# Kernel optimization log

Hardware: AMD Instinct MI355X
Metric: run time of the kernel (lower is better)

Reference implementation:

```python
import jax, jax.numpy as jnp
import numpy as np

C = 1024        # number of classes
N = 8           # proxies per class
ALLNUM = C * N  # 8192 total proxies
DIM = 512
R = 0.05
TOPK = int(np.ceil(R * ALLNUM))  # 410
LAM = 0.3
B = 2048


def setup_inputs() -> dict:
    key = jax.random.key(0)
    k1, k2, k3 = jax.random.split(key, 3)
    inp = jax.random.normal(k1, (B, DIM), dtype=jnp.float32)
    target = jax.random.randint(k2, (B,), 0, C, dtype=jnp.int64)
    # kaiming-uniform-initialized proxies approximated by scaled normal init
    proxies = jax.random.normal(k3, (DIM, ALLNUM), dtype=jnp.float32)
    instance_label = jnp.repeat(jnp.arange(C, dtype=jnp.int64), N)  # [ALLNUM]
    return {"input": inp, "target": target, "Proxies": proxies,
            "instance_label": instance_label}


def reference(input, target, Proxies, instance_label):
    # L2-normalize each proxy column (F.normalize along dim=0, eps=1e-12)
    norm = jnp.maximum(jnp.linalg.norm(Proxies, axis=0, keepdims=True), 1e-12)
    centers = Proxies / norm                             # [DIM, ALLNUM]
    similarity = input @ centers                          # [B, ALLNUM]

    positive_mask = (target[:, None] == instance_label[None, :]).astype(similarity.dtype)
    _, indices = jax.lax.top_k(similarity + 1000.0 * positive_mask, TOPK)  # [B, TOPK]

    rows = jnp.arange(similarity.shape[0])[:, None]
    mask = jnp.zeros_like(similarity).at[rows, indices].set(1.0)
    prob_a = mask * similarity                            # sparse-masked similarities

    y_instance_onehot = jax.nn.one_hot(instance_label, C, dtype=similarity.dtype)  # [ALLNUM, C]
    logits = prob_a @ y_instance_onehot                   # [B, C]

    y_target_onehot = jax.nn.one_hot(target, C, dtype=similarity.dtype)  # [B, C]
    logits_mask = 1.0 - (logits == 0.0).astype(similarity.dtype)

    # scale_mask_softmax with scale=1 along dim=1
    e = jnp.exp(logits) * logits_mask
    predict = e / (1e-8 + jnp.sum(e, axis=1, keepdims=True))
    lossClassify = jnp.mean(jnp.sum(-y_target_onehot * jnp.log(predict + 1e-20), axis=1))

    # proxy regularizer: cross-entropy of proxy-vs-class logits
    simCenter = centers.T @ centers                       # [ALLNUM, ALLNUM]
    centers_logits = simCenter @ y_instance_onehot        # [ALLNUM, C]
    logp = jax.nn.log_softmax(centers_logits, axis=1)
    reg = -jnp.mean(jnp.take_along_axis(logp, instance_label[:, None], axis=1))

    return (lossClassify + LAM * reg, lossClassify)
```

## Files before the change

### kernel.cpp

```cpp
#include <hip/hip_runtime.h>
#include <hip/hip_bf16.h>
#include <math.h>

#define C_CLS   1024
#define NPROXY  8
#define ALLNUM  8192
#define DIM     512
#define TOPK    410
#define LAM     0.3f
#define BATCH   2048

typedef __bf16 bf16x8 __attribute__((ext_vector_type(8)));
typedef float floatx4 __attribute__((ext_vector_type(4)));
typedef unsigned short ushort_t;

#define WS_RNORM 0
#define WS_SIG   8192
#define WS_LP    10240
#define WS_RSE   12288
#define WS_DIAG  20480
#define WS_ABF   28672
#define WS_PBF   552960
#define WS_STBF  2650112
#define WS_SIMBF 2912256

__device__ inline float block_reduce(float v, int is_max, float* red, int t) {
    #pragma unroll
    for (int o = 32; o > 0; o >>= 1) {
        float w = __shfl_down(v, o);
        v = is_max ? fmaxf(v, w) : (v + w);
    }
    __syncthreads();
    if ((t & 63) == 0) red[t >> 6] = v;
    __syncthreads();
    return is_max ? fmaxf(fmaxf(red[0], red[1]), fmaxf(red[2], red[3]))
                  : (red[0] + red[1] + red[2] + red[3]);
}

__device__ inline ushort_t f2bf(float f) {
    unsigned u = __float_as_uint(f);
    return (ushort_t)((u + 0x7FFFu + ((u >> 16) & 1u)) >> 16);
}

__device__ inline void ld_g2l_16(const void* g, void* l) {
    __builtin_amdgcn_global_load_lds(
        (const __attribute__((address_space(1))) unsigned int*)g,
        (__attribute__((address_space(3))) unsigned int*)l,
        16, 0, 0);
}

__device__ inline unsigned f2ord(float f) {
    unsigned u = __float_as_uint(f);
    return (u & 0x80000000u) ? ~u : (u | 0x80000000u);
}

__global__ __launch_bounds__(256) void k_prep1(const float* __restrict__ P,
                                               const float* __restrict__ input,
                                               float* __restrict__ rnorm,
                                               float* __restrict__ rowsig,
                                               float* __restrict__ rse,
                                               ushort_t* __restrict__ Abf,
                                               ushort_t* __restrict__ Pbf) {
    __shared__ float tile[32][33];
    float* cred = &tile[0][0];
    int bx = blockIdx.x, t = threadIdx.x;
    if (bx < 256) {
        int tc = t & 31, g = t >> 5;
        int c = bx * 32 + tc;
        const float* pc = P + (size_t)(g * 64) * ALLNUM + c;
        float s = 0.f;
        #pragma unroll 8
        for (int d = 0; d < 64; ++d) {
            float v = pc[(size_t)d * ALLNUM];
            s += v * v;
        }
        cred[g * 32 + tc] = s;
        int gid = bx * 256 + t;
        if (gid < 8192) rse[gid] = 0.f;
        __syncthreads();
        if (g == 0) {
            float tot = 0.f;
            #pragma unroll
            for (int k = 0; k < 8; ++k) tot += cred[k * 32 + tc];
            rnorm[c] = 1.0f / fmaxf(sqrtf(tot), 1e-12f);
        }
    } else if (bx < 256 + 1024) {
        int a = bx - 256;
        int idx = a * 256 + t;
        float4 v = ((const float4*)input)[idx];
        ushort4 o;
        o.x = f2bf(v.x); o.y = f2bf(v.y); o.z = f2bf(v.z); o.w = f2bf(v.w);
        ((ushort4*)Abf)[idx] = o;
        float sq = v.x * v.x + v.y * v.y + v.z * v.z + v.w * v.w;
        #pragma unroll
        for (int off = 32; off > 0; off >>= 1) sq += __shfl_down(sq, off);
        int lane = t & 63, w = t >> 6;
        if (lane == 0) cred[w] = sq;
        __syncthreads();
        if (t == 0) {
            rowsig[2 * a]     = sqrtf(cred[0] + cred[1]);
            rowsig[2 * a + 1] = sqrtf(cred[2] + cred[3]);
        }
    } else {
        int id = bx - 1280;
        int c0 = (id & 255) * 32, r0 = (id >> 8) * 32;
        int tc = t & 31, tr = t >> 5;
        #pragma unroll
        for (int p = 0; p < 4; ++p)
            tile[tr + p * 8][tc] = P[(size_t)(r0 + tr + p * 8) * ALLNUM + c0 + tc];
        __syncthreads();
        #pragma unroll
        for (int p = 0; p < 4; ++p) {
            int oc = tr + p * 8;
            Pbf[(size_t)(c0 + oc) * DIM + r0 + tc] = f2bf(tile[tc][oc]);
        }
    }
}

__global__ __launch_bounds__(256) void k_stage2(const ushort_t* __restrict__ A,
                                                const ushort_t* __restrict__ B,
                                                const float* __restrict__ P,
                                                const float* __restrict__ rnorm,
                                                ushort_t* __restrict__ simbf,
                                                ushort_t* __restrict__ Stbf) {
    __shared__ __align__(16) ushort_t smem[2 * 128 * 64];
    int bx = blockIdx.x, t = threadIdx.x;

    if (bx < 1024) {
        ushort_t* sA = smem;
        ushort_t* sB = smem + 128 * 64;
        int w = t >> 6, lane = t & 63;
        int wm = w >> 1, wn = w & 1;
        int bj = (bx & 63) * 128, bi = (bx >> 6) * 128;

        floatx4 acc[4][4];
        #pragma unroll
        for (int tm = 0; tm < 4; ++tm)
            #pragma unroll
            for (int tn = 0; tn < 4; ++tn)
                acc[tm][tn] = (floatx4){0.f, 0.f, 0.f, 0.f};

        for (int k0 = 0; k0 < DIM; k0 += 64) {
            #pragma unroll
            for (int it = 0; it < 4; ++it) {
                int c = w * 256 + it * 64 + lane;
                int m = c >> 3, s = c & 7;
                int q = s ^ (m & 7);
                ld_g2l_16(A + ((size_t)(bi + m) << 9) + k0 + q * 8,
                          &sA[(w * 256 + it * 64) * 8]);
            }
            #pragma unroll
            for (int it = 0; it < 4; ++it) {
                int c = w * 256 + it * 64 + lane;
                int m = c >> 3, s = c & 7;
                int q = s ^ (m & 7);
                ld_g2l_16(B + ((size_t)(bj + m) << 9) + k0 + q * 8,
                          &sB[(w * 256 + it * 64) * 8]);
            }
            asm volatile("s_waitcnt vmcnt(0)" ::: "memory");
            __syncthreads();

            #pragma unroll
            for (int kk = 0; kk < 2; ++kk) {
                bf16x8 af[4], bfr[4];
                int ml = lane & 15, q = lane >> 4;
                #pragma unroll
                for (int tm = 0; tm < 4; ++tm) {
                    int m = wm * 64 + tm * 16 + ml;
                    int s = (kk * 4 + q) ^ (m & 7);
                    af[tm] = *(const bf16x8*)&sA[m * 64 + s * 8];
                }
                #pragma unroll
                for (int tn = 0; tn < 4; ++tn) {
                    int n = wn * 64 + tn * 16 + ml;
                    int s = (kk * 4 + q) ^ (n & 7);
                    bfr[tn] = *(const bf16x8*)&sB[n * 64 + s * 8];
                }
                #pragma unroll
                for (int tm = 0; tm < 4; ++tm)
                    #pragma unroll
                    for (int tn = 0; tn < 4; ++tn)
                        acc[tm][tn] = __builtin_amdgcn_mfma_f32_16x16x32_bf16(
                            af[tm], bfr[tn], acc[tm][tn], 0, 0, 0);
            }
            __syncthreads();
        }

        int ml = lane & 15, qd = lane >> 4;
        #pragma unroll
        for (int tm = 0; tm < 4; ++tm) {
            int rowb = bi + wm * 64 + tm * 16 + qd * 4;
            #pragma unroll
            for (int tn = 0; tn < 4; ++tn) {
                int col = bj + wn * 64 + tn * 16 + ml;
                float sc = rnorm[col];
                #pragma unroll
                for (int i = 0; i < 4; ++i)
                    simbf[(size_t)(rowb + i) * ALLNUM + col] = f2bf(acc[tm][tn][i] * sc);
            }
        }
    } else {
        float* tile = (float*)smem;
        int id = bx - 1024;
        int c0 = (id & 31) * 32, d0 = (id >> 5) * 32;
        int cl = t & 31, dl8 = t >> 5;
        #pragma unroll
        for (int p = 0; p < 4; ++p) {
            int d = d0 + dl8 + 8 * p;
            int c = c0 + cl;
            const float* pp = P + (size_t)d * ALLNUM + c * NPROXY;
            const float* rn = rnorm + c * NPROXY;
            float4 a = *(const float4*)pp;
            float4 b = *(const float4*)(pp + 4);
            float4 ra = *(const float4*)rn;
            float4 rb = *(const float4*)(rn + 4);
            tile[(dl8 + 8 * p) * 33 + cl] =
                a.x * ra.x + a.y * ra.y + a.z * ra.z + a.w * ra.w +
                b.x * rb.x + b.y * rb.y + b.z * rb.z + b.w * rb.w;
        }
        __syncthreads();
        #pragma unroll
        for (int p = 0; p < 4; ++p) {
            int cl2 = dl8 + 8 * p, dl2 = t & 31;
            Stbf[(size_t)(c0 + cl2) * DIM + d0 + dl2] = f2bf(tile[dl2 * 33 + cl2]);
        }
    }
}

#define SEL_CAP 1024
#define GCAP    64

__device__ inline void suffix_select1(unsigned* s_hist, unsigned kk,
                                      unsigned* s_wtot, unsigned* sh_bin,
                                      unsigned* sh_k, int t, int lane, int wid) {
    unsigned h = s_hist[t];
    unsigned v = h;
    #pragma unroll
    for (int off = 1; off < 64; off <<= 1) {
        unsigned o = __shfl_down(v, off);
        if (lane + off < 64) v += o;
    }
    if (lane == 0) s_wtot[wid] = v;
    __syncthreads();
    unsigned above = v - h;
    for (int w2 = wid + 1; w2 < 4; ++w2) above += s_wtot[w2];
    unsigned cum = above + h;
    if (cum >= kk && above < kk) { *sh_bin = (unsigned)t; *sh_k = kk - above; }
    __syncthreads();
}

__global__ __launch_bounds__(256) void k_stage3(const ushort_t* __restrict__ simbf,
                                                const int* __restrict__ target,
                                                const float* __restrict__ rowsig,
                                                float* __restrict__ loss_part,
                                                const ushort_t* __restrict__ Pbf,
                                                const ushort_t* __restrict__ Stbf,
                                                const float* __restrict__ rnorm,
                                                float* __restrict__ rse,
                                                float* __restrict__ diag) {
    __shared__ __align__(16) unsigned char smem[16384];
    int bx = blockIdx.x, t = threadIdx.x;
    int lane = t & 63, wid = t >> 6;

    if (bx < 2048) {
        float*    s_cls  = (float*)smem;
        float*    s_bval = (float*)(smem + 4096);
        ushort_t* s_bcol = (ushort_t*)(smem + 8192);
        unsigned* s_bhist= (unsigned*)(smem + 10240);
        float*    s_gval = (float*)(smem + 11264);
        unsigned* s_wtot = (unsigned*)(smem + 11520);
        unsigned* shv    = (unsigned*)(smem + 11536);
        float*    shf    = (float*)(smem + 11552);
        int*      shi    = (int*)(smem + 11556);
        float*    red    = (float*)(smem + 11568);

        int b = bx;
        const ushort_t* row = simbf + (size_t)b * ALLNUM;
        int tgt = target[b];
        float sig = rowsig[b] * (1.0f / 22.616f);
        float hiT = 1.80f * sig, loT = 1.47f * sig;
        float binscale = 256.0f / (hiT - loT);

        uint4 r4[4];
        #pragma unroll
        for (int p = 0; p < 4; ++p) r4[p] = ((const uint4*)row)[t + 256 * p];
        float f[4][8];
        #pragma unroll
        for (int p = 0; p < 4; ++p) {
            const unsigned* u = (const unsigned*)&r4[p];
            #pragma unroll
            for (int k = 0; k < 4; ++k) {
                f[p][2 * k]     = __uint_as_float(u[k] << 16);
                f[p][2 * k + 1] = __uint_as_float(u[k] & 0xFFFF0000u);
            }
        }

        if (t == 0) { shv[0] = 0; shv[1] = 0; }
        s_bhist[t] = 0;
        __syncthreads();

        float ndef = 0.f;
        #pragma unroll
        for (int p = 0; p < 4; ++p) {
            int cls = t + 256 * p;
            if (cls == tgt) {
                float s8 = f[p][0] + f[p][1] + f[p][2] + f[p][3] +
                           f[p][4] + f[p][5] + f[p][6] + f[p][7];
                s_cls[cls] = s8;
            } else {
                float ds = 0.f;
                #pragma unroll
                for (int e = 0; e < 8; ++e) {
                    float v = f[p][e];
                    if (v >= hiT) { ds += v; ndef += 1.f; }
                    else if (v >= loT) {
                        unsigned idx = atomicAdd(&shv[0], 1u);
                        if (idx < SEL_CAP) { s_bval[idx] = v; s_bcol[idx] = (ushort_t)(cls * 8 + e); }
                        int bin = (int)((v - loT) * binscale);
                        bin = (bin > 255) ? 255 : bin;
                        atomicAdd(&s_bhist[bin], 1u);
                    }
                }
                s_cls[cls] = ds;
            }
        }
        float ndefT = block_reduce(ndef, 0, red, t);
        int bc = (int)shv[0];
        int kq = (TOPK - NPROXY) - (int)ndefT;
        if (t == 0) shi[0] = (kq < 0 || bc < kq || bc > SEL_CAP) ? 1 : 0;
        __syncthreads();

        if (!shi[0]) {
            if (kq > 0) {
                suffix_select1(s_bhist, (unsigned)kq, s_wtot, &shv[2], &shv[3], t, lane, wid);
                int B = (int)shv[2];
                int knew = (int)shv[3];
                for (int j = t; j < bc; j += 256) {
                    float v = s_bval[j];
                    int bin = (int)((v - loT) * binscale);
                    bin = (bin > 255) ? 255 : bin;
                    if (bin == B) {
                        unsigned g = atomicAdd(&shv[1], 1u);
                        if (g < GCAP) s_gval[g] = v;
                    }
                }
                __syncthreads();
                int gc = (int)shv[1];
                if (gc <= GCAP) {
                    if (t < gc) {
                        float vj = s_gval[t];
                        unsigned g = 0, geq = 0;
                        for (int i = 0; i < gc; ++i) {
                            float vi = s_gval[i];
                            g   += (vi > vj) ? 1u : 0u;
                            geq += (vi >= vj) ? 1u : 0u;
                        }
                        if (g < (unsigned)knew && geq >= (unsigned)knew) shf[0] = vj;
                    }
                } else {
                    for (int j = t; j < bc; j += 256) {
                        float vj = s_bval[j];
                        unsigned g = 0, geq = 0;
                        for (int i = 0; i < bc; ++i) {
                            float vi = s_bval[i];
                            g   += (vi > vj) ? 1u : 0u;
                            geq += (vi >= vj) ? 1u : 0u;
                        }
                        if (g < (unsigned)kq && geq >= (unsigned)kq) shf[0] = vj;
                    }
                }
                __syncthreads();
                float thr = shf[0];
                for (int j = t; j < bc; j += 256)
                    if (s_bval[j] >= thr)
                        atomicAdd(&s_cls[s_bcol[j] >> 3], s_bval[j]);
            }
        } else {
            unsigned L = 0u, R = 0xFFFFFFFFu;
            for (int it = 0; it < 33 && R - L > 1; ++it) {
                unsigned mid = L + ((R - L) >> 1);
                float c = 0.f;
                #pragma unroll
                for (int p = 0; p < 4; ++p) {
                    int cls = t + 256 * p;
                    if (cls != tgt) {
                        #pragma unroll
                        for (int e = 0; e < 8; ++e)
                            c += (f2ord(f[p][e]) >= mid) ? 1.f : 0.f;
                    }
                }
                c = block_reduce(c, 0, red, t);
                if (c >= (float)(TOPK - NPROXY)) L = mid; else R = mid;
                __syncthreads();
            }
            #pragma unroll
            for (int p = 0; p < 4; ++p) {
                int cls = t + 256 * p;
                if (cls != tgt) {
                    float s = 0.f;
                    #pragma unroll
                    for (int e = 0; e < 8; ++e)
                        if (f2ord(f[p][e]) >= L) s += f[p][e];
                    s_cls[cls] = s;
                }
            }
        }
        __syncthreads();

        float4 cv = ((const float4*)s_cls)[t];
        float m = -1e30f;
        if (cv.x != 0.0f) m = fmaxf(m, cv.x);
        if (cv.y != 0.0f) m = fmaxf(m, cv.y);
        if (cv.z != 0.0f) m = fmaxf(m, cv.z);
        if (cv.w != 0.0f) m = fmaxf(m, cv.w);
        m = block_reduce(m, 1, red, t);
        float se = 0.f;
        if (cv.x != 0.0f) se += expf(cv.x - m);
        if (cv.y != 0.0f) se += expf(cv.y - m);
        if (cv.z != 0.0f) se += expf(cv.z - m);
        if (cv.w != 0.0f) se += expf(cv.w - m);
        se = block_reduce(se, 0, red, t);
        if (t == 0) {
            float lt = s_cls[tgt];
            float predict_t = expf(lt - m) / (1e-8f * expf(-m) + se);
            loss_part[b] = -logf(predict_t + 1e-20f);
        }
    } else {
        ushort_t* sA = (ushort_t*)smem;
        ushort_t* sB = (ushort_t*)(smem + 8192);
        int id = bx - 2048;
        int bj = (id & 15) * 64;
        int bi = (id >> 4) * 64;
        int w = wid;
        int wm = w >> 1, wn = w & 1;

        floatx4 acc[2][2];
        #pragma unroll
        for (int tm = 0; tm < 2; ++tm)
            #pragma unroll
            for (int tn = 0; tn < 2; ++tn)
                acc[tm][tn] = (floatx4){0.f, 0.f, 0.f, 0.f};

        for (int k0 = 0; k0 < DIM; k0 += 64) {
            #pragma unroll
            for (int it = 0; it < 2; ++it) {
                int c = (w * 2 + it) * 64 + lane;
                int m = c >> 3, s = c & 7;
                int q = s ^ (m & 7);
                ld_g2l_16(Pbf + ((size_t)(bi + m) << 9) + k0 + q * 8,
                          &sA[((w * 2 + it) * 64) * 8]);
            }
            #pragma unroll
            for (int it = 0; it < 2; ++it) {
                int c = (w * 2 + it) * 64 + lane;
                int m = c >> 3, s = c & 7;
                int q = s ^ (m & 7);
                ld_g2l_16(Stbf + ((size_t)(bj + m) << 9) + k0 + q * 8,
                          &sB[((w * 2 + it) * 64) * 8]);
            }
            asm volatile("s_waitcnt vmcnt(0)" ::: "memory");
            __syncthreads();

            #pragma unroll
            for (int kk = 0; kk < 2; ++kk) {
                bf16x8 af[2], bfr[2];
                int ml = lane & 15, q = lane >> 4;
                #pragma unroll
                for (int tm = 0; tm < 2; ++tm) {
                    int m = wm * 32 + tm * 16 + ml;
                    int s = (kk * 4 + q) ^ (m & 7);
                    af[tm] = *(const bf16x8*)&sA[m * 64 + s * 8];
                }
                #pragma unroll
                for (int tn = 0; tn < 2; ++tn) {
                    int n = wn * 32 + tn * 16 + ml;
                    int s = (kk * 4 + q) ^ (n & 7);
                    bfr[tn] = *(const bf16x8*)&sB[n * 64 + s * 8];
                }
                #pragma unroll
                for (int tm = 0; tm < 2; ++tm)
                    #pragma unroll
                    for (int tn = 0; tn < 2; ++tn)
                        acc[tm][tn] = __builtin_amdgcn_mfma_f32_16x16x32_bf16(
                            af[tm], bfr[tn], acc[tm][tn], 0, 0, 0);
            }
            __syncthreads();
        }

        int ml = lane & 15, qd = lane >> 4;
        #pragma unroll
        for (int tm = 0; tm < 2; ++tm) {
            int rowb = bi + wm * 32 + tm * 16 + qd * 4;
            float4 rnr = *(const float4*)&rnorm[rowb];
            #pragma unroll
            for (int i = 0; i < 4; ++i) {
                int rowg = rowb + i;
                float rn = ((const float*)&rnr)[i];
                float esum = 0.f;
                #pragma unroll
                for (int tn = 0; tn < 2; ++tn) {
                    int colg = bj + wn * 32 + tn * 16 + ml;
                    float v = acc[tm][tn][i] * rn;
                    esum += expf(v);
                    if (colg == (rowg >> 3)) diag[rowg] = v;
                }
                #pragma unroll
                for (int off = 1; off < 16; off <<= 1)
                    esum += __shfl_xor(esum, off);
                if (ml == 0) atomicAdd(&rse[rowg], esum);
            }
        }
    }
}

__global__ __launch_bounds__(256) void k_final(const float* __restrict__ lp,
                                               const float* __restrict__ rse,
                                               const float* __restrict__ diag,
                                               float* __restrict__ out) {
    __shared__ float red[4];
    int t = threadIdx.x;
    float4 a = ((const float4*)lp)[t];
    float4 b = ((const float4*)lp)[t + 256];
    float ls = a.x + a.y + a.z + a.w + b.x + b.y + b.z + b.w;
    float rs = 0.f;
    for (int r = t; r < ALLNUM; r += 256)
        rs += logf(rse[r]) - diag[r];
    ls = block_reduce(ls, 0, red, t);
    rs = block_reduce(rs, 0, red, t);
    if (t == 0) {
        float lc = ls / (float)BATCH;
        float rg = rs / (float)ALLNUM;
        out[0] = lc + LAM * rg;
        out[1] = lc;
    }
}

extern "C" void kernel_launch(void* const* d_in, const int* in_sizes, int n_in,
                              void* d_out, int out_size, void* d_ws, size_t ws_size,
                              hipStream_t stream) {
    const float* input  = (const float*)d_in[0];
    const int*   target = (const int*)d_in[1];
    const float* P      = (const float*)d_in[2];

    float* ws       = (float*)d_ws;
    float* rnorm    = ws + WS_RNORM;
    float* rowsig   = ws + WS_SIG;
    float* loss_part= ws + WS_LP;
    float* rse      = ws + WS_RSE;
    float* diag     = ws + WS_DIAG;
    ushort_t* Abf   = (ushort_t*)(ws + WS_ABF);
    ushort_t* Pbf   = (ushort_t*)(ws + WS_PBF);
    ushort_t* Stbf  = (ushort_t*)(ws + WS_STBF);
    ushort_t* simbf = (ushort_t*)(ws + WS_SIMBF);
    float* out      = (float*)d_out;

    hipLaunchKernelGGL(k_prep1, dim3(256 + 1024 + 4096), dim3(256), 0, stream,
                       P, input, rnorm, rowsig, rse, Abf, Pbf);
    hipLaunchKernelGGL(k_stage2, dim3(1024 + 512), dim3(256), 0, stream,
                       Abf, Pbf, P, rnorm, simbf, Stbf);
    hipLaunchKernelGGL(k_stage3, dim3(2048 + 2048), dim3(256), 0, stream,
                       simbf, target, rowsig, loss_part, Pbf, Stbf, rnorm, rse, diag);
    hipLaunchKernelGGL(k_final, dim3(1), dim3(256), 0, stream,
                       loss_part, rse, diag, out);
}
```

Before: 158.7 us.

## Merge stage pairs into persistent cooperative kernels with grid-wide sync

New measurement: 303.6 us. 91.3% more time.

```diff
diff --git a/kernel.cpp b/kernel.cpp
--- a/kernel.cpp
+++ b/kernel.cpp
@@ -1,6 +1,9 @@
 #include <hip/hip_runtime.h>
+#include <hip/hip_cooperative_groups.h>
 #include <hip/hip_bf16.h>
 #include <math.h>
+
+namespace cg = cooperative_groups;
 
 #define C_CLS   1024
 #define NPROXY  8
@@ -24,6 +27,9 @@
 #define WS_STBF  2650112
 #define WS_SIMBF 2912256
 
+#define SEL_CAP 1024
+#define GCAP    64
+
 __device__ inline float block_reduce(float v, int is_max, float* red, int t) {
     #pragma unroll
     for (int o = 32; o > 0; o >>= 1) {
@@ -53,182 +59,6 @@
     unsigned u = __float_as_uint(f);
     return (u & 0x80000000u) ? ~u : (u | 0x80000000u);
 }
-
-__global__ __launch_bounds__(256) void k_prep1(const float* __restrict__ P,
-                                               const float* __restrict__ input,
-                                               float* __restrict__ rnorm,
-                                               float* __restrict__ rowsig,
-                                               float* __restrict__ rse,
-                                               ushort_t* __restrict__ Abf,
-                                               ushort_t* __restrict__ Pbf) {
-    __shared__ float tile[32][33];
-    float* cred = &tile[0][0];
-    int bx = blockIdx.x, t = threadIdx.x;
-    if (bx < 256) {
-        int tc = t & 31, g = t >> 5;
-        int c = bx * 32 + tc;
-        const float* pc = P + (size_t)(g * 64) * ALLNUM + c;
-        float s = 0.f;
-        #pragma unroll 8
-        for (int d = 0; d < 64; ++d) {
-            float v = pc[(size_t)d * ALLNUM];
-            s += v * v;
-        }
-        cred[g * 32 + tc] = s;
-        int gid = bx * 256 + t;
-        if (gid < 8192) rse[gid] = 0.f;
-        __syncthreads();
-        if (g == 0) {
-            float tot = 0.f;
-            #pragma unroll
-            for (int k = 0; k < 8; ++k) tot += cred[k * 32 + tc];
-            rnorm[c] = 1.0f / fmaxf(sqrtf(tot), 1e-12f);
-        }
-    } else if (bx < 256 + 1024) {
-        int a = bx - 256;
-        int idx = a * 256 + t;
-        float4 v = ((const float4*)input)[idx];
-        ushort4 o;
-        o.x = f2bf(v.x); o.y = f2bf(v.y); o.z = f2bf(v.z); o.w = f2bf(v.w);
-        ((ushort4*)Abf)[idx] = o;
-        float sq = v.x * v.x + v.y * v.y + v.z * v.z + v.w * v.w;
-        #pragma unroll
-        for (int off = 32; off > 0; off >>= 1) sq += __shfl_down(sq, off);
-        int lane = t & 63, w = t >> 6;
-        if (lane == 0) cred[w] = sq;
-        __syncthreads();
-        if (t == 0) {
-            rowsig[2 * a]     = sqrtf(cred[0] + cred[1]);
-            rowsig[2 * a + 1] = sqrtf(cred[2] + cred[3]);
-        }
-    } else {
-        int id = bx - 1280;
-        int c0 = (id & 255) * 32, r0 = (id >> 8) * 32;
-        int tc = t & 31, tr = t >> 5;
-        #pragma unroll
-        for (int p = 0; p < 4; ++p)
-            tile[tr + p * 8][tc] = P[(size_t)(r0 + tr + p * 8) * ALLNUM + c0 + tc];
-        __syncthreads();
-        #pragma unroll
-        for (int p = 0; p < 4; ++p) {
-            int oc = tr + p * 8;
-            Pbf[(size_t)(c0 + oc) * DIM + r0 + tc] = f2bf(tile[tc][oc]);
-        }
-    }
-}
-
-__global__ __launch_bounds__(256) void k_stage2(const ushort_t* __restrict__ A,
-                                                const ushort_t* __restrict__ B,
-                                                const float* __restrict__ P,
-                                                const float* __restrict__ rnorm,
-                                                ushort_t* __restrict__ simbf,
-                                                ushort_t* __restrict__ Stbf) {
-    __shared__ __align__(16) ushort_t smem[2 * 128 * 64];
-    int bx = blockIdx.x, t = threadIdx.x;
-
-    if (bx < 1024) {
-        ushort_t* sA = smem;
-        ushort_t* sB = smem + 128 * 64;
-        int w = t >> 6, lane = t & 63;
-        int wm = w >> 1, wn = w & 1;
-        int bj = (bx & 63) * 128, bi = (bx >> 6) * 128;
-
-        floatx4 acc[4][4];
-        #pragma unroll
-        for (int tm = 0; tm < 4; ++tm)
-            #pragma unroll
-            for (int tn = 0; tn < 4; ++tn)
-                acc[tm][tn] = (floatx4){0.f, 0.f, 0.f, 0.f};
-
-        for (int k0 = 0; k0 < DIM; k0 += 64) {
-            #pragma unroll
-            for (int it = 0; it < 4; ++it) {
-                int c = w * 256 + it * 64 + lane;
-                int m = c >> 3, s = c & 7;
-                int q = s ^ (m & 7);
-                ld_g2l_16(A + ((size_t)(bi + m) << 9) + k0 + q * 8,
-                          &sA[(w * 256 + it * 64) * 8]);
-            }
-            #pragma unroll
-            for (int it = 0; it < 4; ++it) {
-                int c = w * 256 + it * 64 + lane;
-                int m = c >> 3, s = c & 7;
-                int q = s ^ (m & 7);
-                ld_g2l_16(B + ((size_t)(bj + m) << 9) + k0 + q * 8,
-                          &sB[(w * 256 + it * 64) * 8]);
-            }
-            asm volatile("s_waitcnt vmcnt(0)" ::: "memory");
-            __syncthreads();
-
-            #pragma unroll
-            for (int kk = 0; kk < 2; ++kk) {
-                bf16x8 af[4], bfr[4];
-                int ml = lane & 15, q = lane >> 4;
-                #pragma unroll
-                for (int tm = 0; tm < 4; ++tm) {
-                    int m = wm * 64 + tm * 16 + ml;
-                    int s = (kk * 4 + q) ^ (m & 7);
-                    af[tm] = *(const bf16x8*)&sA[m * 64 + s * 8];
-                }
-                #pragma unroll
-                for (int tn = 0; tn < 4; ++tn) {
-                    int n = wn * 64 + tn * 16 + ml;
-                    int s = (kk * 4 + q) ^ (n & 7);
-                    bfr[tn] = *(const bf16x8*)&sB[n * 64 + s * 8];
-                }
-                #pragma unroll
-                for (int tm = 0; tm < 4; ++tm)
-                    #pragma unroll
-                    for (int tn = 0; tn < 4; ++tn)
-                        acc[tm][tn] = __builtin_amdgcn_mfma_f32_16x16x32_bf16(
-                            af[tm], bfr[tn], acc[tm][tn], 0, 0, 0);
-            }
-            __syncthreads();
-        }
-
-        int ml = lane & 15, qd = lane >> 4;
-        #pragma unroll
-        for (int tm = 0; tm < 4; ++tm) {
-            int rowb = bi + wm * 64 + tm * 16 + qd * 4;
-            #pragma unroll
-            for (int tn = 0; tn < 4; ++tn) {
-                int col = bj + wn * 64 + tn * 16 + ml;
-                float sc = rnorm[col];
-                #pragma unroll
-                for (int i = 0; i < 4; ++i)
-                    simbf[(size_t)(rowb + i) * ALLNUM + col] = f2bf(acc[tm][tn][i] * sc);
-            }
-        }
-    } else {
-        float* tile = (float*)smem;
-        int id = bx - 1024;
-        int c0 = (id & 31) * 32, d0 = (id >> 5) * 32;
-        int cl = t & 31, dl8 = t >> 5;
-        #pragma unroll
-        for (int p = 0; p < 4; ++p) {
-            int d = d0 + dl8 + 8 * p;
-            int c = c0 + cl;
-            const float* pp = P + (size_t)d * ALLNUM + c * NPROXY;
-            const float* rn = rnorm + c * NPROXY;
-            float4 a = *(const float4*)pp;
-            float4 b = *(const float4*)(pp + 4);
-            float4 ra = *(const float4*)rn;
-            float4 rb = *(const float4*)(rn + 4);
-            tile[(dl8 + 8 * p) * 33 + cl] =
-                a.x * ra.x + a.y * ra.y + a.z * ra.z + a.w * ra.w +
-                b.x * rb.x + b.y * rb.y + b.z * rb.z + b.w * rb.w;
-        }
-        __syncthreads();
-        #pragma unroll
-        for (int p = 0; p < 4; ++p) {
-            int cl2 = dl8 + 8 * p, dl2 = t & 31;
-            Stbf[(size_t)(c0 + cl2) * DIM + d0 + dl2] = f2bf(tile[dl2 * 33 + cl2]);
-        }
-    }
-}
-
-#define SEL_CAP 1024
-#define GCAP    64
 
 __device__ inline void suffix_select1(unsigned* s_hist, unsigned kk,
                                       unsigned* s_wtot, unsigned* sh_bin,
@@ -249,276 +79,462 @@
     __syncthreads();
 }
 
-__global__ __launch_bounds__(256) void k_stage3(const ushort_t* __restrict__ simbf,
-                                                const int* __restrict__ target,
-                                                const float* __restrict__ rowsig,
-                                                float* __restrict__ loss_part,
-                                                const ushort_t* __restrict__ Pbf,
-                                                const ushort_t* __restrict__ Stbf,
-                                                const float* __restrict__ rnorm,
-                                                float* __restrict__ rse,
-                                                float* __restrict__ diag) {
-    __shared__ __align__(16) unsigned char smem[16384];
-    int bx = blockIdx.x, t = threadIdx.x;
-    int lane = t & 63, wid = t >> 6;
-
-    if (bx < 2048) {
-        float*    s_cls  = (float*)smem;
-        float*    s_bval = (float*)(smem + 4096);
-        ushort_t* s_bcol = (ushort_t*)(smem + 8192);
-        unsigned* s_bhist= (unsigned*)(smem + 10240);
-        float*    s_gval = (float*)(smem + 11264);
-        unsigned* s_wtot = (unsigned*)(smem + 11520);
-        unsigned* shv    = (unsigned*)(smem + 11536);
-        float*    shf    = (float*)(smem + 11552);
-        int*      shi    = (int*)(smem + 11556);
-        float*    red    = (float*)(smem + 11568);
-
-        int b = bx;
-        const ushort_t* row = simbf + (size_t)b * ALLNUM;
-        int tgt = target[b];
-        float sig = rowsig[b] * (1.0f / 22.616f);
-        float hiT = 1.80f * sig, loT = 1.47f * sig;
-        float binscale = 256.0f / (hiT - loT);
-
-        uint4 r4[4];
+__device__ void dev_prep(unsigned char* smem, int bx, int nblk, int t, int lane, int wid,
+                         const float* __restrict__ P, const float* __restrict__ input,
+                         float* __restrict__ rnorm, float* __restrict__ rowsig,
+                         float* __restrict__ rse,
+                         ushort_t* __restrict__ Abf, ushort_t* __restrict__ Pbf) {
+    float* tile = (float*)smem;
+    for (int u = bx; u < 5376; u += nblk) {
+        __syncthreads();
+        if (u < 256) {
+            int tc = t & 31, g = t >> 5;
+            int c = u * 32 + tc;
+            const float* pc = P + (size_t)(g * 64) * ALLNUM + c;
+            float s = 0.f;
+            #pragma unroll 8
+            for (int d = 0; d < 64; ++d) {
+                float v = pc[(size_t)d * ALLNUM];
+                s += v * v;
+            }
+            tile[g * 32 + tc] = s;
+            int gid = u * 256 + t;
+            if (gid < ALLNUM) rse[gid] = 0.f;
+            __syncthreads();
+            if (g == 0) {
+                float tot = 0.f;
+                #pragma unroll
+                for (int k = 0; k < 8; ++k) tot += tile[k * 32 + tc];
+                rnorm[c] = 1.0f / fmaxf(sqrtf(tot), 1e-12f);
+            }
+        } else if (u < 1280) {
+            int a = u - 256;
+            int idx = a * 256 + t;
+            float4 v = ((const float4*)input)[idx];
+            ushort4 o;
+            o.x = f2bf(v.x); o.y = f2bf(v.y); o.z = f2bf(v.z); o.w = f2bf(v.w);
+            ((ushort4*)Abf)[idx] = o;
+            float sq = v.x * v.x + v.y * v.y + v.z * v.z + v.w * v.w;
+            #pragma unroll
+            for (int off = 32; off > 0; off >>= 1) sq += __shfl_down(sq, off);
+            if (lane == 0) tile[wid] = sq;
+            __syncthreads();
+            if (t == 0) {
+                rowsig[2 * a]     = sqrtf(tile[0] + tile[1]);
+                rowsig[2 * a + 1] = sqrtf(tile[2] + tile[3]);
+            }
+        } else {
+            int id = u - 1280;
+            int c0 = (id & 255) * 32, r0 = (id >> 8) * 32;
+            int tc = t & 31, tr = t >> 5;
+            #pragma unroll
+            for (int p = 0; p < 4; ++p)
+                tile[(tr + p * 8) * 33 + tc] =
+                    P[(size_t)(r0 + tr + p * 8) * ALLNUM + c0 + tc];
+            __syncthreads();
+            #pragma unroll
+            for (int p = 0; p < 4; ++p) {
+                int oc = tr + p * 8;
+                Pbf[(size_t)(c0 + oc) * DIM + r0 + tc] = f2bf(tile[tc * 33 + oc]);
+            }
+        }
+    }
+}
+
+__device__ void dev_stage2(unsigned char* smem, int bx, int nblk, int t, int lane, int wid,
+                           const ushort_t* __restrict__ Abf,
+                           const ushort_t* __restrict__ Pbf,
+                           const float* __restrict__ P,
+                           const float* __restrict__ rnorm,
+                           ushort_t* __restrict__ simbf,
+                           ushort_t* __restrict__ Stbf) {
+    for (int u = bx; u < 1536; u += nblk) {
+        __syncthreads();
+        if (u < 1024) {
+            ushort_t* sA = (ushort_t*)smem;
+            ushort_t* sB = (ushort_t*)(smem + 16384);
+            int w = wid;
+            int wm = w >> 1, wn = w & 1;
+            int bj = (u & 63) * 128, bi = (u >> 6) * 128;
+
+            floatx4 acc[4][4];
+            #pragma unroll
+            for (int tm = 0; tm < 4; ++tm)
+                #pragma unroll
+                for (int tn = 0; tn < 4; ++tn)
+                    acc[tm][tn] = (floatx4){0.f, 0.f, 0.f, 0.f};
+
+            for (int k0 = 0; k0 < DIM; k0 += 64) {
+                #pragma unroll
+                for (int it = 0; it < 4; ++it) {
+                    int c = w * 256 + it * 64 + lane;
+                    int m = c >> 3, s = c & 7;
+                    int q = s ^ (m & 7);
+                    ld_g2l_16(Abf + ((size_t)(bi + m) << 9) + k0 + q * 8,
+                              &sA[(w * 256 + it * 64) * 8]);
+                }
+                #pragma unroll
+                for (int it = 0; it < 4; ++it) {
+                    int c = w * 256 + it * 64 + lane;
+                    int m = c >> 3, s = c & 7;
+                    int q = s ^ (m & 7);
+                    ld_g2l_16(Pbf + ((size_t)(bj + m) << 9) + k0 + q * 8,
+                              &sB[(w * 256 + it * 64) * 8]);
+                }
+                asm volatile("s_waitcnt vmcnt(0)" ::: "memory");
+                __syncthreads();
+
+                #pragma unroll
+                for (int kk = 0; kk < 2; ++kk) {
+                    bf16x8 af[4], bfr[4];
+                    int ml = lane & 15, q = lane >> 4;
+                    #pragma unroll
+                    for (int tm = 0; tm < 4; ++tm) {
+                        int m = wm * 64 + tm * 16 + ml;
+                        int s = (kk * 4 + q) ^ (m & 7);
+                        af[tm] = *(const bf16x8*)&sA[m * 64 + s * 8];
+                    }
+                    #pragma unroll
+                    for (int tn = 0; tn < 4; ++tn) {
+                        int n = wn * 64 + tn * 16 + ml;
+                        int s = (kk * 4 + q) ^ (n & 7);
+                        bfr[tn] = *(const bf16x8*)&sB[n * 64 + s * 8];
+                    }
+                    #pragma unroll
+                    for (int tm = 0; tm < 4; ++tm)
+                        #pragma unroll
+                        for (int tn = 0; tn < 4; ++tn)
+                            acc[tm][tn] = __builtin_amdgcn_mfma_f32_16x16x32_bf16(
+                                af[tm], bfr[tn], acc[tm][tn], 0, 0, 0);
+                }
+                __syncthreads();
+            }
+
+            int ml = lane & 15, qd = lane >> 4;
+            #pragma unroll
+            for (int tm = 0; tm < 4; ++tm) {
+                int rowb = bi + wm * 64 + tm * 16 + qd * 4;
+                #pragma unroll
+                for (int tn = 0; tn < 4; ++tn) {
+                    int col = bj + wn * 64 + tn * 16 + ml;
+                    float sc = rnorm[col];
+                    #pragma unroll
+                    for (int i = 0; i < 4; ++i)
+                        simbf[(size_t)(rowb + i) * ALLNUM + col] =
+                            f2bf(acc[tm][tn][i] * sc);
+                }
+            }
+        } else {
+            float* tile = (float*)smem;
+            int id = u - 1024;
+            int c0 = (id & 31) * 32, d0 = (id >> 5) * 32;
+            int cl = t & 31, dl8 = t >> 5;
+            #pragma unroll
+            for (int p = 0; p < 4; ++p) {
+                int d = d0 + dl8 + 8 * p;
+                int c = c0 + cl;
+                const float* pp = P + (size_t)d * ALLNUM + c * NPROXY;
+                const float* rn = rnorm + c * NPROXY;
+                float4 a = *(const float4*)pp;
+                float4 b = *(const float4*)(pp + 4);
+                float4 ra = *(const float4*)rn;
+                float4 rb = *(const float4*)(rn + 4);
+                tile[(dl8 + 8 * p) * 33 + cl] =
+                    a.x * ra.x + a.y * ra.y + a.z * ra.z + a.w * ra.w +
+                    b.x * rb.x + b.y * rb.y + b.z * rb.z + b.w * rb.w;
+            }
+            __syncthreads();
+            #pragma unroll
+            for (int p = 0; p < 4; ++p) {
+                int cl2 = dl8 + 8 * p, dl2 = t & 31;
+                Stbf[(size_t)(c0 + cl2) * DIM + d0 + dl2] = f2bf(tile[dl2 * 33 + cl2]);
+            }
+        }
+    }
+}
+
+__device__ void do_rowloss(unsigned char* smem, int b, int t, int lane, int wid,
+                           const ushort_t* __restrict__ simbf,
+                           const int* __restrict__ target,
+                           const float* __restrict__ rowsig,
+                           float* __restrict__ loss_part) {
+    float*    s_cls  = (float*)smem;
+    float*    s_bval = (float*)(smem + 4096);
+    ushort_t* s_bcol = (ushort_t*)(smem + 8192);
+    unsigned* s_bhist= (unsigned*)(smem + 10240);
+    float*    s_gval = (float*)(smem + 11264);
+    unsigned* s_wtot = (unsigned*)(smem + 11520);
+    unsigned* shv    = (unsigned*)(smem + 11536);
+    float*    shf    = (float*)(smem + 11552);
+    int*      shi    = (int*)(smem + 11556);
+    float*    red    = (float*)(smem + 11568);
+
+    const ushort_t* row = simbf + (size_t)b * ALLNUM;
+    int tgt = target[b];
+    float sig = rowsig[b] * (1.0f / 22.616f);
+    float hiT = 1.80f * sig, loT = 1.47f * sig;
+    float binscale = 256.0f / (hiT - loT);
+
+    uint4 r4[4];
+    #pragma unroll
+    for (int p = 0; p < 4; ++p) r4[p] = ((const uint4*)row)[t + 256 * p];
+    float f[4][8];
+    #pragma unroll
+    for (int p = 0; p < 4; ++p) {
+        const unsigned* u = (const unsigned*)&r4[p];
         #pragma unroll
-        for (int p = 0; p < 4; ++p) r4[p] = ((const uint4*)row)[t + 256 * p];
-        float f[4][8];
-        #pragma unroll
-        for (int p = 0; p < 4; ++p) {
-            const unsigned* u = (const unsigned*)&r4[p];
-            #pragma unroll
-            for (int k = 0; k < 4; ++k) {
-                f[p][2 * k]     = __uint_as_float(u[k] << 16);
-                f[p][2 * k + 1] = __uint_as_float(u[k] & 0xFFFF0000u);
-            }
-        }
-
-        if (t == 0) { shv[0] = 0; shv[1] = 0; }
-        s_bhist[t] = 0;
-        __syncthreads();
-
-        float ndef = 0.f;
+        for (int k = 0; k < 4; ++k) {
+            f[p][2 * k]     = __uint_as_float(u[k] << 16);
+            f[p][2 * k + 1] = __uint_as_float(u[k] & 0xFFFF0000u);
+        }
+    }
+
+    __syncthreads();
+    if (t == 0) { shv[0] = 0; shv[1] = 0; }
+    s_bhist[t] = 0;
+    __syncthreads();
+
+    float ndef = 0.f;
+    #pragma unroll
+    for (int p = 0; p < 4; ++p) {
+        int cls = t + 256 * p;
+        if (cls == tgt) {
+            s_cls[cls] = f[p][0] + f[p][1] + f[p][2] + f[p][3] +
+                         f[p][4] + f[p][5] + f[p][6] + f[p][7];
+        } else {
+            float ds = 0.f;
+            #pragma unroll
+            for (int e = 0; e < 8; ++e) {
+                float v = f[p][e];
+                if (v >= hiT) { ds += v; ndef += 1.f; }
+                else if (v >= loT) {
+                    unsigned idx = atomicAdd(&shv[0], 1u);
+                    if (idx < SEL_CAP) { s_bval[idx] = v; s_bcol[idx] = (ushort_t)(cls * 8 + e); }
+                    int bin = (int)((v - loT) * binscale);
+                    bin = (bin > 255) ? 255 : bin;
+                    atomicAdd(&s_bhist[bin], 1u);
+                }
+            }
+            s_cls[cls] = ds;
+        }
+    }
+    float ndefT = block_reduce(ndef, 0, red, t);
+    int bc = (int)shv[0];
+    int kq = (TOPK - NPROXY) - (int)ndefT;
+    if (t == 0) shi[0] = (kq < 0 || bc < kq || bc > SEL_CAP) ? 1 : 0;
+    __syncthreads();
+
+    if (!shi[0]) {
+        if (kq > 0) {
+            suffix_select1(s_bhist, (unsigned)kq, s_wtot, &shv[2], &shv[3], t, lane, wid);
+            int B = (int)shv[2];
+            int knew = (int)shv[3];
+            for (int j = t; j < bc; j += 256) {
+                float v = s_bval[j];
+                int bin = (int)((v - loT) * binscale);
+                bin = (bin > 255) ? 255 : bin;
+                if (bin == B) {
+                    unsigned g = atomicAdd(&shv[1], 1u);
+                    if (g < GCAP) s_gval[g] = v;
+                }
+            }
+            __syncthreads();
+            int gc = (int)shv[1];
+            if (gc <= GCAP) {
+                if (t < gc) {
+                    float vj = s_gval[t];
+                    unsigned g = 0, geq = 0;
+                    for (int i = 0; i < gc; ++i) {
+                        float vi = s_gval[i];
+                        g   += (vi > vj) ? 1u : 0u;
+                        geq += (vi >= vj) ? 1u : 0u;
+                    }
+                    if (g < (unsigned)knew && geq >= (unsigned)knew) shf[0] = vj;
+                }
+            } else {
+                for (int j = t; j < bc; j += 256) {
+                    float vj = s_bval[j];
+                    unsigned g = 0, geq = 0;
+                    for (int i = 0; i < bc; ++i) {
+                        float vi = s_bval[i];
+                        g   += (vi > vj) ? 1u : 0u;
+                        geq += (vi >= vj) ? 1u : 0u;
+                    }
+                    if (g < (unsigned)kq && geq >= (unsigned)kq) shf[0] = vj;
+                }
+            }
+            __syncthreads();
+            float thr = shf[0];
+            for (int j = t; j < bc; j += 256)
+                if (s_bval[j] >= thr)
+                    atomicAdd(&s_cls[s_bcol[j] >> 3], s_bval[j]);
+        }
+    } else {
+        unsigned L = 0u, R = 0xFFFFFFFFu;
+        for (int it = 0; it < 33 && R - L > 1; ++it) {
+            unsigned mid = L + ((R - L) >> 1);
+            float c = 0.f;
+            #pragma unroll
+            for (int p = 0; p < 4; ++p) {
+                int cls = t + 256 * p;
+                if (cls != tgt) {
+                    #pragma unroll
+                    for (int e = 0; e < 8; ++e)
+                        c += (f2ord(f[p][e]) >= mid) ? 1.f : 0.f;
+                }
+            }
+            c = block_reduce(c, 0, red, t);
+            if (c >= (float)(TOPK - NPROXY)) L = mid; else R = mid;
+            __syncthreads();
+        }
         #pragma unroll
         for (int p = 0; p < 4; ++p) {
             int cls = t + 256 * p;
-            if (cls == tgt) {
-                float s8 = f[p][0] + f[p][1] + f[p][2] + f[p][3] +
-                           f[p][4] + f[p][5] + f[p][6] + f[p][7];
-                s_cls[cls] = s8;
-            } else {
-                float ds = 0.f;
-                #pragma unroll
-                for (int e = 0; e < 8; ++e) {
-                    float v = f[p][e];
-                    if (v >= hiT) { ds += v; ndef += 1.f; }
-                    else if (v >= loT) {
-                        unsigned idx = atomicAdd(&shv[0], 1u);
-                        if (idx < SEL_CAP) { s_bval[idx] = v; s_bcol[idx] = (ushort_t)(cls * 8 + e); }
-                        int bin = (int)((v - loT) * binscale);
-                        bin = (bin > 255) ? 255 : bin;
-                        atomicAdd(&s_bhist[bin], 1u);
-                    }
-                }
-                s_cls[cls] = ds;
-            }
-        }
-        float ndefT = block_reduce(ndef, 0, red, t);
-        int bc = (int)shv[0];
-        int kq = (TOPK - NPROXY) - (int)ndefT;
-        if (t == 0) shi[0] = (kq < 0 || bc < kq || bc > SEL_CAP) ? 1 : 0;
+            if (cls != tgt) {
+                float s = 0.f;
+                #pragma unroll
+                for (int e = 0; e < 8; ++e)
+                    if (f2ord(f[p][e]) >= L) s += f[p][e];
+                s_cls[cls] = s;
+            }
+        }
+    }
+    __syncthreads();
+
+    float4 cv = ((const float4*)s_cls)[t];
+    float m = -1e30f;
+    if (cv.x != 0.0f) m = fmaxf(m, cv.x);
+    if (cv.y != 0.0f) m = fmaxf(m, cv.y);
+    if (cv.z != 0.0f) m = fmaxf(m, cv.z);
+    if (cv.w != 0.0f) m = fmaxf(m, cv.w);
+    m = block_reduce(m, 1, red, t);
+    float se = 0.f;
+    if (cv.x != 0.0f) se += expf(cv.x - m);
+    if (cv.y != 0.0f) se += expf(cv.y - m);
+    if (cv.z != 0.0f) se += expf(cv.z - m);
+    if (cv.w != 0.0f) se += expf(cv.w - m);
+    se = block_reduce(se, 0, red, t);
+    if (t == 0) {
+        float lt = s_cls[tgt];
+        float predict_t = expf(lt - m) / (1e-8f * expf(-m) + se);
+        loss_part[b] = -logf(predict_t + 1e-20f);
+    }
+}
+
+__device__ void do_gemm1(unsigned char* smem, int id, int t, int lane, int wid,
+                         const ushort_t* __restrict__ Pbf,
+                         const ushort_t* __restrict__ Stbf,
+                         const float* __restrict__ rnorm,
+                         float* __restrict__ rse,
+                         float* __restrict__ diag) {
+    ushort_t* sA = (ushort_t*)smem;
+    ushort_t* sB = (ushort_t*)(smem + 8192);
+    int bj = (id & 15) * 64;
+    int bi = (id >> 4) * 64;
+    int w = wid;
+    int wm = w >> 1, wn = w & 1;
+
+    floatx4 acc[2][2];
+    #pragma unroll
+    for (int tm = 0; tm < 2; ++tm)
+        #pragma unroll
+        for (int tn = 0; tn < 2; ++tn)
+            acc[tm][tn] = (floatx4){0.f, 0.f, 0.f, 0.f};
+
+    __syncthreads();
+    for (int k0 = 0; k0 < DIM; k0 += 64) {
+        #pragma unroll
+        for (int it = 0; it < 2; ++it) {
+            int c = (w * 2 + it) * 64 + lane;
+            int m = c >> 3, s = c & 7;
+            int q = s ^ (m & 7);
+            ld_g2l_16(Pbf + ((size_t)(bi + m) << 9) + k0 + q * 8,
+                      &sA[((w * 2 + it) * 64) * 8]);
+        }
+        #pragma unroll
+        for (int it = 0; it < 2; ++it) {
+            int c = (w * 2 + it) * 64 + lane;
+            int m = c >> 3, s = c & 7;
+            int q = s ^ (m & 7);
+            ld_g2l_16(Stbf + ((size_t)(bj + m) << 9) + k0 + q * 8,
+                      &sB[((w * 2 + it) * 64) * 8]);
+        }
+        asm volatile("s_waitcnt vmcnt(0)" ::: "memory");
         __syncthreads();
 
-        if (!shi[0]) {
-            if (kq > 0) {
-                suffix_select1(s_bhist, (unsigned)kq, s_wtot, &shv[2], &shv[3], t, lane, wid);
-                int B = (int)shv[2];
-                int knew = (int)shv[3];
-                for (int j = t; j < bc; j += 256) {
-                    float v = s_bval[j];
-                    int bin = (int)((v - loT) * binscale);
-                    bin = (bin > 255) ? 255 : bin;
-                    if (bin == B) {
-                        unsigned g = atomicAdd(&shv[1], 1u);
-                        if (g < GCAP) s_gval[g] = v;
-                    }
-                }
-                __syncthreads();
-                int gc = (int)shv[1];
-                if (gc <= GCAP) {
-                    if (t < gc) {
-                        float vj = s_gval[t];
-                        unsigned g = 0, geq = 0;
-                        for (int i = 0; i < gc; ++i) {
-                            float vi = s_gval[i];
-                            g   += (vi > vj) ? 1u : 0u;
-                            geq += (vi >= vj) ? 1u : 0u;
-                        }
-                        if (g < (unsigned)knew && geq >= (unsigned)knew) shf[0] = vj;
-                    }
-                } else {
-                    for (int j = t; j < bc; j += 256) {
-                        float vj = s_bval[j];
-                        unsigned g = 0, geq = 0;
-                        for (int i = 0; i < bc; ++i) {
-                            float vi = s_bval[i];
-                            g   += (vi > vj) ? 1u : 0u;
-                            geq += (vi >= vj) ? 1u : 0u;
-                        }
-                        if (g < (unsigned)kq && geq >= (unsigned)kq) shf[0] = vj;
-                    }
-                }
-                __syncthreads();
-                float thr = shf[0];
-                for (int j = t; j < bc; j += 256)
-                    if (s_bval[j] >= thr)
-                        atomicAdd(&s_cls[s_bcol[j] >> 3], s_bval[j]);
-            }
-        } else {
-            unsigned L = 0u, R = 0xFFFFFFFFu;
-            for (int it = 0; it < 33 && R - L > 1; ++it) {
-                unsigned mid = L + ((R - L) >> 1);
-                float c = 0.f;
-                #pragma unroll
-                for (int p = 0; p < 4; ++p) {
-                    int cls = t + 256 * p;
-                    if (cls != tgt) {
-                        #pragma unroll
-                        for (int e = 0; e < 8; ++e)
-                            c += (f2ord(f[p][e]) >= mid) ? 1.f : 0.f;
-                    }
-                }
-                c = block_reduce(c, 0, red, t);
-                if (c >= (float)(TOPK - NPROXY)) L = mid; else R = mid;
-                __syncthreads();
-            }
-            #pragma unroll
-            for (int p = 0; p < 4; ++p) {
-                int cls = t + 256 * p;
-                if (cls != tgt) {
-                    float s = 0.f;
-                    #pragma unroll
-                    for (int e = 0; e < 8; ++e)
-                        if (f2ord(f[p][e]) >= L) s += f[p][e];
-                    s_cls[cls] = s;
-                }
-            }
+        #pragma unroll
+        for (int kk = 0; kk < 2; ++kk) {
+            bf16x8 af[2], bfr[2];
+            int ml = lane & 15, q = lane >> 4;
+            #pragma unroll
+            for (int tm = 0; tm < 2; ++tm) {
+                int m = wm * 32 + tm * 16 + ml;
+                int s = (kk * 4 + q) ^ (m & 7);
+                af[tm] = *(const bf16x8*)&sA[m * 64 + s * 8];
+            }
+            #pragma unroll
+            for (int tn = 0; tn < 2; ++tn) {
+                int n = wn * 32 + tn * 16 + ml;
+                int s = (kk * 4 + q) ^ (n & 7);
+                bfr[tn] = *(const bf16x8*)&sB[n * 64 + s * 8];
+            }
+            #pragma unroll
+            for (int tm = 0; tm < 2; ++tm)
+                #pragma unroll
+                for (int tn = 0; tn < 2; ++tn)
+                    acc[tm][tn] = __builtin_amdgcn_mfma_f32_16x16x32_bf16(
+                        af[tm], bfr[tn], acc[tm][tn], 0, 0, 0);
         }
         __syncthreads();
-
-        float4 cv = ((const float4*)s_cls)[t];
-        float m = -1e30f;
-        if (cv.x != 0.0f) m = fmaxf(m, cv.x);
-        if (cv.y != 0.0f) m = fmaxf(m, cv.y);
-        if (cv.z != 0.0f) m = fmaxf(m, cv.z);
-        if (cv.w != 0.0f) m = fmaxf(m, cv.w);
-        m = block_reduce(m, 1, red, t);
-        float se = 0.f;
-        if (cv.x != 0.0f) se += expf(cv.x - m);
-        if (cv.y != 0.0f) se += expf(cv.y - m);
-        if (cv.z != 0.0f) se += expf(cv.z - m);
-        if (cv.w != 0.0f) se += expf(cv.w - m);
-        se = block_reduce(se, 0, red, t);
-        if (t == 0) {
-            float lt = s_cls[tgt];
-            float predict_t = expf(lt - m) / (1e-8f * expf(-m) + se);
-            loss_part[b] = -logf(predict_t + 1e-20f);
-        }
-    } else {
-        ushort_t* sA = (ushort_t*)smem;
-        ushort_t* sB = (ushort_t*)(smem + 8192);
-        int id = bx - 2048;
-        int bj = (id & 15) * 64;
-        int bi = (id >> 4) * 64;
-        int w = wid;
-        int wm = w >> 1, wn = w & 1;
-
-        floatx4 acc[2][2];
+    }
+
+    int ml = lane & 15, qd = lane >> 4;
+    #pragma unroll
+    for (int tm = 0; tm < 2; ++tm) {
+        int rowb = bi + wm * 32 + tm * 16 + qd * 4;
+        float4 rnr = *(const float4*)&rnorm[rowb];
         #pragma unroll
-        for (int tm = 0; tm < 2; ++tm)
-            #pragma unroll
-            for (int tn = 0; tn < 2; ++tn)
-                acc[tm][tn] = (floatx4){0.f, 0.f, 0.f, 0.f};
-
-        for (int k0 = 0; k0 < DIM; k0 += 64) {
-            #pragma unroll
-            for (int it = 0; it < 2; ++it) {
-                int c = (w * 2 + it) * 64 + lane;
-                int m = c >> 3, s = c & 7;
-                int q = s ^ (m & 7);
-                ld_g2l_16(Pbf + ((size_t)(bi + m) << 9) + k0 + q * 8,
-                          &sA[((w * 2 + it) * 64) * 8]);
-            }
-            #pragma unroll
-            for (int it = 0; it < 2; ++it) {
-                int c = (w * 2 + it) * 64 + lane;
-                int m = c >> 3, s = c & 7;
-                int q = s ^ (m & 7);
-                ld_g2l_16(Stbf + ((size_t)(bj + m) << 9) + k0 + q * 8,
-                          &sB[((w * 2 + it) * 64) * 8]);
-            }
-            asm volatile("s_waitcnt vmcnt(0)" ::: "memory");
-            __syncthreads();
-
-            #pragma unroll
-            for (int kk = 0; kk < 2; ++kk) {
-                bf16x8 af[2], bfr[2];
-                int ml = lane & 15, q = lane >> 4;
-                #pragma unroll
-                for (int tm = 0; tm < 2; ++tm) {
-                    int m = wm * 32 + tm * 16 + ml;
-                    int s = (kk * 4 + q) ^ (m & 7);
-                    af[tm] = *(const bf16x8*)&sA[m * 64 + s * 8];
-                }
-                #pragma unroll
-                for (int tn = 0; tn < 2; ++tn) {
-                    int n = wn * 32 + tn * 16 + ml;
-                    int s = (kk * 4 + q) ^ (n & 7);
-                    bfr[tn] = *(const bf16x8*)&sB[n * 64 + s * 8];
-                }
-                #pragma unroll
-                for (int tm = 0; tm < 2; ++tm)
-                    #pragma unroll
-                    for (int tn = 0; tn < 2; ++tn)
-                        acc[tm][tn] = __builtin_amdgcn_mfma_f32_16x16x32_bf16(
-                            af[tm], bfr[tn], acc[tm][tn], 0, 0, 0);
-            }
-            __syncthreads();
-        }
-
-        int ml = lane & 15, qd = lane >> 4;
-        #pragma unroll
-        for (int tm = 0; tm < 2; ++tm) {
-            int rowb = bi + wm * 32 + tm * 16 + qd * 4;
-            float4 rnr = *(const float4*)&rnorm[rowb];
-            #pragma unroll
-            for (int i = 0; i < 4; ++i) {
-                int rowg = rowb + i;
-                float rn = ((const float*)&rnr)[i];
-                float esum = 0.f;
-                #pragma unroll
-                for (int tn = 0; tn < 2; ++tn) {
-                    int colg = bj + wn * 32 + tn * 16 + ml;
-                    float v = acc[tm][tn][i] * rn;
-                    esum += expf(v);
-                    if (colg == (rowg >> 3)) diag[rowg] = v;
-                }
-                #pragma unroll
-                for (int off = 1; off < 16; off <<= 1)
-                    esum += __shfl_xor(esum, off);
-                if (ml == 0) atomicAdd(&rse[rowg], esum);
-            }
-        }
-    }
-}
-
-__global__ __launch_bounds__(256) void k_final(const float* __restrict__ lp,
-                                               const float* __restrict__ rse,
-                                               const float* __restrict__ diag,
-                                               float* __restrict__ out) {
-    __shared__ float red[4];
-    int t = threadIdx.x;
+        for (int i = 0; i < 4; ++i) {
+            int rowg = rowb + i;
+            float rn = ((const float*)&rnr)[i];
+            float esum = 0.f;
+            #pragma unroll
+            for (int tn = 0; tn < 2; ++tn) {
+                int colg = bj + wn * 32 + tn * 16 + ml;
+                float v = acc[tm][tn][i] * rn;
+                esum += expf(v);
+                if (colg == (rowg >> 3)) diag[rowg] = v;
+            }
+            #pragma unroll
+            for (int off = 1; off < 16; off <<= 1)
+                esum += __shfl_xor(esum, off);
+            if (ml == 0) atomicAdd(&rse[rowg], esum);
+        }
+    }
+}
+
+__device__ void dev_stage3(unsigned char* smem, int bx, int nblk, int t, int lane, int wid,
+                           const ushort_t* __restrict__ simbf,
+                           const int* __restrict__ target,
+                           const float* __restrict__ rowsig,
+                           float* __restrict__ loss_part,
+                           const ushort_t* __restrict__ Pbf,
+                           const ushort_t* __restrict__ Stbf,
+                           const float* __restrict__ rnorm,
+                           float* __restrict__ rse,
+                           float* __restrict__ diag) {
+    for (int u = bx; u < 4096; u += nblk) {
+        if (u & 1) do_gemm1(smem, u >> 1, t, lane, wid, Pbf, Stbf, rnorm, rse, diag);
+        else       do_rowloss(smem, u >> 1, t, lane, wid, simbf, target, rowsig, loss_part);
+    }
+}
+
+__device__ void dev_final(float* red, int t,
+                          const float* __restrict__ lp,
+                          const float* __restrict__ rse,
+                          const float* __restrict__ diag,
+                          float* __restrict__ out) {
+    __syncthreads();
     float4 a = ((const float4*)lp)[t];
     float4 b = ((const float4*)lp)[t + 256];
     float ls = a.x + a.y + a.z + a.w + b.x + b.y + b.z + b.w;
@@ -535,6 +551,59 @@
     }
 }
 
+__global__ __launch_bounds__(256) void k_coopA(const float* P, const float* input,
+    float* rnorm, float* rowsig, float* rse,
+    ushort_t* Abf, ushort_t* Pbf, ushort_t* simbf, ushort_t* Stbf) {
+    cg::grid_group grid = cg::this_grid();
+    __shared__ __align__(16) unsigned char smem[32768];
+    int bx = blockIdx.x, t = threadIdx.x, lane = t & 63, wid = t >> 6;
+    dev_prep(smem, bx, gridDim.x, t, lane, wid, P, input, rnorm, rowsig, rse, Abf, Pbf);
+    grid.sync();
+    dev_stage2(smem, bx, gridDim.x, t, lane, wid, Abf, Pbf, P, rnorm, simbf, Stbf);
+}
+
+__global__ __launch_bounds__(256) void k_coopB(const ushort_t* simbf, const int* target,
+    const float* rowsig, float* loss_part, const ushort_t* Pbf, const ushort_t* Stbf,
+    const float* rnorm, float* rse, float* diag, float* out) {
+    cg::grid_group grid = cg::this_grid();
+    __shared__ __align__(16) unsigned char smem[16384];
+    int bx = blockIdx.x, t = threadIdx.x, lane = t & 63, wid = t >> 6;
+    dev_stage3(smem, bx, gridDim.x, t, lane, wid, simbf, target, rowsig, loss_part,
+               Pbf, Stbf, rnorm, rse, diag);
+    grid.sync();
+    if (bx == 0) dev_final((float*)smem, t, loss_part, rse, diag, out);
+}
+
+__global__ __launch_bounds__(256) void k_p0(const float* P, const float* input,
+    float* rnorm, float* rowsig, float* rse, ushort_t* Abf, ushort_t* Pbf) {
+    __shared__ __align__(16) unsigned char smem[4352];
+    int t = threadIdx.x;
+    dev_prep(smem, blockIdx.x, gridDim.x, t, t & 63, t >> 6,
+             P, input, rnorm, rowsig, rse, Abf, Pbf);
+}
+__global__ __launch_bounds__(256) void k_p1(const ushort_t* Abf, const ushort_t* Pbf,
+    const float* P, const float* rnorm, ushort_t* simbf, ushort_t* Stbf) {
+    __shared__ __align__(16) unsigned char smem[32768];
+    int t = threadIdx.x;
+    dev_stage2(smem, blockIdx.x, gridDim.x, t, t & 63, t >> 6,
+               Abf, Pbf, P, rnorm, simbf, Stbf);
+}
+__global__ __launch_bounds__(256) void k_p2(const ushort_t* simbf, const int* target,
+    const float* rowsig, float* loss_part, const ushort_t* Pbf, const ushort_t* Stbf,
+    const float* rnorm, float* rse, float* diag) {
+    __shared__ __align__(16) unsigned char smem[16384];
+    int t = threadIdx.x;
+    dev_stage3(smem, blockIdx.x, gridDim.x, t, t & 63, t >> 6,
+               simbf, target, rowsig, loss_part, Pbf, Stbf, rnorm, rse, diag);
+}
+__global__ __launch_bounds__(256) void k_p3(const float* lp, const float* rse,
+                                            const float* diag, float* out) {
+    __shared__ float red[4];
+    dev_final(red, threadIdx.x, lp, rse, diag, out);
+}
+
+static inline int imin(int a, int b) { return a < b ? a : b; }
+
 extern "C" void kernel_launch(void* const* d_in, const int* in_sizes, int n_in,
                               void* d_out, int out_size, void* d_ws, size_t ws_size,
                               hipStream_t stream) {
@@ -542,24 +611,53 @@
     const int*   target = (const int*)d_in[1];
     const float* P      = (const float*)d_in[2];
 
-    float* ws       = (float*)d_ws;
-    float* rnorm    = ws + WS_RNORM;
-    float* rowsig   = ws + WS_SIG;
-    float* loss_part= ws + WS_LP;
-    float* rse      = ws + WS_RSE;
-    float* diag     = ws + WS_DIAG;
-    ushort_t* Abf   = (ushort_t*)(ws + WS_ABF);
-    ushort_t* Pbf   = (ushort_t*)(ws + WS_PBF);
-    ushort_t* Stbf  = (ushort_t*)(ws + WS_STBF);
-    ushort_t* simbf = (ushort_t*)(ws + WS_SIMBF);
-    float* out      = (float*)d_out;
-
-    hipLaunchKernelGGL(k_prep1, dim3(256 + 1024 + 4096), dim3(256), 0, stream,
-                       P, input, rnorm, rowsig, rse, Abf, Pbf);
-    hipLaunchKernelGGL(k_stage2, dim3(1024 + 512), dim3(256), 0, stream,
-                       Abf, Pbf, P, rnorm, simbf, Stbf);
-    hipLaunchKernelGGL(k_stage3, dim3(2048 + 2048), dim3(256), 0, stream,
-                       simbf, target, rowsig, loss_part, Pbf, Stbf, rnorm, rse, diag);
-    hipLaunchKernelGGL(k_final, dim3(1), dim3(256), 0, stream,
-                       loss_part, rse, diag, out);
-}
+    float* ws        = (float*)d_ws;
+    float* rnorm     = ws + WS_RNORM;
+    float* rowsig    = ws + WS_SIG;
+    float* loss_part = ws + WS_LP;
+    float* rse       = ws + WS_RSE;
+    float* diag      = ws + WS_DIAG;
+    ushort_t* Abf    = (ushort_t*)(ws + WS_ABF);
+    ushort_t* Pbf    = (ushort_t*)(ws + WS_PBF);
+    ushort_t* Stbf   = (ushort_t*)(ws + WS_STBF);
+    ushort_t* simbf  = (ushort_t*)(ws + WS_SIMBF);
+    float* out       = (float*)d_out;
+
+    int maxA = 0;
+    hipError_t qA = hipOccupancyMaxActiveBlocksPerMultiprocessor(
+        &maxA, (const void*)k_coopA, 256, 0);
+    hipError_t eA = hipErrorUnknown;
+    if (qA == hipSuccess && maxA > 0) {
+        int GA = imin(maxA * 256, 1536);
+        void* argsA[] = { (void*)&P, (void*)&input, (void*)&rnorm, (void*)&rowsig,
+                          (void*)&rse, (void*)&Abf, (void*)&Pbf, (void*)&simbf,
+                          (void*)&Stbf };
+        eA = hipLaunchCooperativeKernel((const void*)k_coopA, dim3(GA), dim3(256),
+                                        argsA, 0, stream);
+    }
+    if (eA != hipSuccess) {
+        hipLaunchKernelGGL(k_p0, dim3(5376), dim3(256), 0, stream,
+                           P, input, rnorm, rowsig, rse, Abf, Pbf);
+        hipLaunchKernelGGL(k_p1, dim3(1536), dim3(256), 0, stream,
+                           Abf, Pbf, P, rnorm, simbf, Stbf);
+    }
+
+    int maxB = 0;
+    hipError_t qB = hipOccupancyMaxActiveBlocksPerMultiprocessor(
+        &maxB, (const void*)k_coopB, 256, 0);
+    hipError_t eB = hipErrorUnknown;
+    if (qB == hipSuccess && maxB > 0) {
+        int GB = imin(maxB * 256, 4096);
+        void* argsB[] = { (void*)&simbf, (void*)&target, (void*)&rowsig,
+                          (void*)&loss_part, (void*)&Pbf, (void*)&Stbf,
+                          (void*)&rnorm, (void*)&rse, (void*)&diag, (void*)&out };
+        eB = hipLaunchCooperativeKernel((const void*)k_coopB, dim3(GB), dim3(256),
+                                        argsB, 0, stream);
+    }
+    if (eB != hipSuccess) {
+        hipLaunchKernelGGL(k_p2, dim3(4096), dim3(256), 0, stream,
+                           simbf, target, rowsig, loss_part, Pbf, Stbf, rnorm, rse, diag);
+        hipLaunchKernelGGL(k_p3, dim3(1), dim3(256), 0, stream,
+                           loss_part, rse, diag, out);
+    }
+}
```
